# Kernel tuning notes

Measured on AMD Instinct MI355X. Metric: run time of the kernel, lower is better.

## Reference

```python
import jax, jax.numpy as jnp
import numpy as np

DX, DZ, DT = 10.0, 10.0, 1.0e-3
NX, NZ = 512, 512
NSTEPS, NREC = 512, 128
DT2 = DT * DT
INV_DXDZ = 1.0 / (DX * DZ)


def setup_inputs() -> dict:
    key = jax.random.key(0)
    k1, k2, k3, k4 = jax.random.split(key, 4)
    # velocity in [1500, 2500] m/s -> CFL stable with dt=1e-3, dx=dz=10
    velocity_model = 1500.0 + 1000.0 * jax.random.uniform(k1, (NX, NZ), dtype=jnp.float32)
    source = jax.random.normal(k2, (NSTEPS,), dtype=jnp.float32)
    rec_x = jax.random.randint(k3, (NREC,), 0, NX)
    rec_z = jax.random.randint(k4, (NREC,), 0, NZ)
    return {
        "velocity_model": velocity_model,
        "source": source,
        "src_x": 256,
        "src_z": 8,
        "rec_x": rec_x,
        "rec_z": rec_z,
    }


def _laplacian(p):
    # 3x3 cross stencil with zero padding, scaled by 1/(dx*dz) -- identical to
    # F.conv2d(p, [[0,1,0],[1,-4,1],[0,1,0]]/(dx*dz), padding=1)
    pp = jnp.pad(p, 1)
    return (pp[:-2, 1:-1] + pp[2:, 1:-1] + pp[1:-1, :-2] + pp[1:-1, 2:] - 4.0 * p) * INV_DXDZ


def reference(velocity_model, source, src_x, src_z, rec_x, rec_z):
    v2_dt2 = velocity_model * velocity_model * DT2  # [nx, nz]

    def step(carry, s_t):
        p, p_old = carry
        p_new = 2.0 * p - p_old + v2_dt2 * _laplacian(p)
        p_new = p_new.at[src_x, src_z].add(s_t * DT2)
        return (p_new, p), p_new[rec_x, rec_z]  # gather all receivers at once

    p0 = jnp.zeros((NX, NZ), dtype=velocity_model.dtype)
    _, recs = jax.lax.scan(step, (p0, p0), source)  # recs: [n_steps, n_rec]
    return recs.T  # seismogram: [n_rec, n_steps]
```

## Files before the change

kernel.cpp:

```cpp
#include <hip/hip_runtime.h>


#define NXd 512
#define NZd 512
#define NSTEPSd 512
#define NRECd 128
#define DT2f 1.0e-6f
#define INVf 1.0e-2f
#define TBk 16
#define TIk 32
#define EXTk 64
#define NTILEk 16
#define PADk 16
#define PWk 544
#define LROWS 66

__device__ __forceinline__ float dpp_shr1(float x) {
    int v = __builtin_amdgcn_update_dpp(0, __builtin_bit_cast(int, x),
                                        0x138, 0xF, 0xF, false);
    return __builtin_bit_cast(float, v);
}
__device__ __forceinline__ float dpp_shl1(float x) {
    int v = __builtin_amdgcn_update_dpp(0, __builtin_bit_cast(int, x),
                                        0x130, 0xF, 0xF, false);
    return __builtin_bit_cast(float, v);
}

__global__ __launch_bounds__(256) void fdtd_init(const float* __restrict__ vel,
                                                 float2* __restrict__ PA,
                                                 float2* __restrict__ PB,
                                                 float* __restrict__ V2,
                                                 float* __restrict__ out) {
    int p = blockIdx.x * blockDim.x + threadIdx.x;
    if (p < PWk * PWk) {
        int px = p / PWk, pz = p - px * PWk;
        float v2 = 0.f;
        if (px >= PADk && px < PADk + NXd && pz >= PADk && pz < PADk + NZd) {
            float v = vel[(px - PADk) * NZd + (pz - PADk)];
            v2 = v * v * (DT2f * INVf);
        }
        PA[p] = make_float2(0.f, 0.f);
        PB[p] = make_float2(0.f, 0.f);
        V2[p] = v2;
    }
    if (p < NRECd * NSTEPSd) out[p] = 0.f;
}

__global__ __launch_bounds__(1024) void fdtd_tblock(
    const float* __restrict__ source,
    const int* __restrict__ src_x, const int* __restrict__ src_z,
    const int* __restrict__ rec_x, const int* __restrict__ rec_z,
    const float2* __restrict__ Pin, float2* __restrict__ Pout,
    const float* __restrict__ V2, float* __restrict__ out,
    int t0, int ibase)
{
    __shared__ float sb[2][LROWS * EXTk];

    const int tid = threadIdx.x;
    const int w   = tid >> 6;
    const int ez  = tid & 63;
    const int gx0 = (blockIdx.y + ibase) * TIk;
    const int gz0 = blockIdx.x * TIk;
    const int ox = gx0 - TBk, oz = gz0 - TBk;
    const int gz = oz + ez;

    const int pbase = (gx0 + 4 * w) * PWk + gz0 + ez;
    float2 co[4]; float rV2i[4];
    #pragma unroll
    for (int i = 0; i < 4; ++i) {
        co[i]   = Pin[pbase + i * PWk];
        rV2i[i] = V2[pbase + i * PWk];
    }

    const int sx = *src_x, sz = *src_z;
    {
        int dxm = max(0, max(ox - sx, sx - (ox + EXTk - 1)));
        int dzm = max(0, max(oz - sz, sz - (oz + EXTk - 1)));
        if (dxm + dzm > t0 + TBk + 1) return;
    }

    bool rOwn = false; int rIdx = 0;
    if (tid < NRECd) {
        int rx = rec_x[tid], rz = rec_z[tid];
        rOwn = (rx >= gx0 && rx < gx0 + TIk && rz >= gz0 && rz < gz0 + TIk);
        rIdx = (rx - ox + 1) * EXTk + (rz - oz);
    }

    float rCur[4], rOld[4];
    #pragma unroll
    for (int i = 0; i < 4; ++i) {
        rCur[i] = co[i].x; rOld[i] = co[i].y;
        sb[0][(4 * w + 1 + i) * EXTk + ez] = rCur[i];
    }
    if (w == 0) {
        sb[0][ez] = 0.f;
        sb[0][(LROWS - 1) * EXTk + ez] = 0.f;
        sb[1][ez] = 0.f;
        sb[1][(LROWS - 1) * EXTk + ez] = 0.f;
    }

    const int exs = sx - ox, ezs = sz - oz;
    const bool srcHere = (exs >= 0 && exs < EXTk && ezs >= 0 && ezs < EXTk) &&
                         (tid == (((exs >> 2) << 6) | ezs));
    float sv[TBk];
    if (srcHere) {
        #pragma unroll
        for (int s = 0; s < TBk; ++s) sv[s] = source[t0 + s] * DT2f;
    }

    __syncthreads();

    const int fbase = 4 * w * EXTk + ez;

    float rv[TBk];
    #pragma unroll
    for (int s = 0; s < TBk; ++s) {
        const float* cur = sb[s & 1];
        float* nxt = sb[(s & 1) ^ 1];
        const float up0 = cur[fbase];
        const float dn3 = cur[fbase + 5 * EXTk];
        float nv[4];
        #pragma unroll
        for (int i = 0; i < 4; ++i) {
            const float up = (i == 0) ? up0 : rCur[i - 1];
            const float dn = (i == 3) ? dn3 : rCur[i + 1];
            const float lf = dpp_shr1(rCur[i]);
            const float rt = dpp_shl1(rCur[i]);
            const float sum = (up + dn) + (lf + rt);
            const float t4 = __builtin_fmaf(-4.0f, rCur[i], sum);
            const float pm = __builtin_fmaf(2.0f, rCur[i], -rOld[i]);
            nv[i] = __builtin_fmaf(rV2i[i], t4, pm);
        }
        #pragma unroll
        for (int i = 0; i < 4; ++i) {
            rOld[i] = rCur[i];
            rCur[i] = nv[i];
            nxt[fbase + (1 + i) * EXTk] = nv[i];
        }
        if (srcHere) {
            #pragma unroll
            for (int i = 0; i < 4; ++i) {
                if (i == (exs & 3)) {
                    rCur[i] += sv[s];
                    nxt[(exs + 1) * EXTk + ezs] = rCur[i];
                }
            }
        }
        __syncthreads();
        if (rOwn) rv[s] = nxt[rIdx];
    }

    if (w >= 4 && w < 12 && ez >= TBk && ez < EXTk - TBk) {
        #pragma unroll
        for (int i = 0; i < 4; ++i)
            Pout[pbase + i * PWk] = make_float2(rCur[i], rOld[i]);
    }

    if (rOwn) {
        #pragma unroll
        for (int s = 0; s < TBk; ++s)
            out[tid * NSTEPSd + t0 + s] = rv[s];
    }
}

extern "C" void kernel_launch(void* const* d_in, const int* in_sizes, int n_in,
                              void* d_out, int out_size, void* d_ws, size_t ws_size,
                              hipStream_t stream) {
    const float* vel    = (const float*)d_in[0];
    const float* source = (const float*)d_in[1];
    const int*   src_x  = (const int*)d_in[2];
    const int*   src_z  = (const int*)d_in[3];
    const int*   rec_x  = (const int*)d_in[4];
    const int*   rec_z  = (const int*)d_in[5];
    float* out = (float*)d_out;

    const size_t FP = (size_t)PWk * PWk;
    float2* PA = (float2*)d_ws;
    float2* PB = PA + FP;
    float*  V2 = (float*)(PB + FP);

    fdtd_init<<<(PWk * PWk + 255) / 256, 256, 0, stream>>>(vel, PA, PB, V2, out);

    for (int k = 0; k < NSTEPSd / TBk; ++k) {
        const int R = 16 * k + TBk + 1 + 32;
        const int tneg = 209 - R;
        int ilo = tneg > 0 ? (tneg + 31) / 32 : 0;
        int ihi = (272 + R) / 32; if (ihi > 15) ihi = 15;
        int jhi = (24 + R) / 32;  if (jhi > 15) jhi = 15;

        const float2* Pin = (k & 1) ? PB : PA;
        float2* Pout      = (k & 1) ? PA : PB;
        dim3 grid(jhi + 1, ihi - ilo + 1);
        fdtd_tblock<<<grid, dim3(1024), 0, stream>>>(source, src_x, src_z,
                                                     rec_x, rec_z, Pin, Pout,
                                                     V2, out, 16 * k, ilo);
    }
}
```

Baseline: 362.3 us.

## Replace per-chunk launches with a persistent cooperative kernel using grid sync

```diff
diff --git a/kernel.cpp b/kernel.cpp
--- a/kernel.cpp
+++ b/kernel.cpp
@@ -1,4 +1,7 @@
 #include <hip/hip_runtime.h>
+#include <hip/hip_cooperative_groups.h>
+
+namespace cg = cooperative_groups;
 
 
 #define NXd 512
@@ -26,58 +29,59 @@
     return __builtin_bit_cast(float, v);
 }
 
-__global__ __launch_bounds__(256) void fdtd_init(const float* __restrict__ vel,
-                                                 float2* __restrict__ PA,
-                                                 float2* __restrict__ PB,
-                                                 float* __restrict__ V2,
-                                                 float* __restrict__ out) {
-    int p = blockIdx.x * blockDim.x + threadIdx.x;
-    if (p < PWk * PWk) {
-        int px = p / PWk, pz = p - px * PWk;
-        float v2 = 0.f;
-        if (px >= PADk && px < PADk + NXd && pz >= PADk && pz < PADk + NZd) {
-            float v = vel[(px - PADk) * NZd + (pz - PADk)];
-            v2 = v * v * (DT2f * INVf);
-        }
-        PA[p] = make_float2(0.f, 0.f);
-        PB[p] = make_float2(0.f, 0.f);
-        V2[p] = v2;
-    }
-    if (p < NRECd * NSTEPSd) out[p] = 0.f;
-}
-
-__global__ __launch_bounds__(1024) void fdtd_tblock(
-    const float* __restrict__ source,
+__global__ __launch_bounds__(1024) void fdtd_persist(
+    const float* __restrict__ vel, const float* __restrict__ source,
     const int* __restrict__ src_x, const int* __restrict__ src_z,
     const int* __restrict__ rec_x, const int* __restrict__ rec_z,
-    const float2* __restrict__ Pin, float2* __restrict__ Pout,
-    const float* __restrict__ V2, float* __restrict__ out,
-    int t0, int ibase)
+    float2* __restrict__ PA, float2* __restrict__ PB,
+    float* __restrict__ out)
 {
+    cg::grid_group gg = cg::this_grid();
     __shared__ float sb[2][LROWS * EXTk];
 
     const int tid = threadIdx.x;
     const int w   = tid >> 6;
     const int ez  = tid & 63;
-    const int gx0 = (blockIdx.y + ibase) * TIk;
+    const int gx0 = blockIdx.y * TIk;
     const int gz0 = blockIdx.x * TIk;
     const int ox = gx0 - TBk, oz = gz0 - TBk;
-    const int gz = oz + ez;
-
-    const int pbase = (gx0 + 4 * w) * PWk + gz0 + ez;
-    float2 co[4]; float rV2i[4];
-    #pragma unroll
-    for (int i = 0; i < 4; ++i) {
-        co[i]   = Pin[pbase + i * PWk];
-        rV2i[i] = V2[pbase + i * PWk];
+
+    {
+        const int gsz = (int)(gridDim.x * gridDim.y) * (int)blockDim.x;
+        int g = ((int)(blockIdx.y * gridDim.x + blockIdx.x)) * (int)blockDim.x + tid;
+        for (int p = g; p < PWk * PWk; p += gsz) {
+            PA[p] = make_float2(0.f, 0.f);
+            PB[p] = make_float2(0.f, 0.f);
+        }
+        if (g < NRECd * NSTEPSd) out[g] = 0.f;
+    }
+
+    float rV2i[4];
+    {
+        const int fz = oz + ez;
+        #pragma unroll
+        for (int i = 0; i < 4; ++i) {
+            const int fx = ox + 4 * w + i;
+            float v2 = 0.f;
+            if (fx >= 0 && fx < NXd && fz >= 0 && fz < NZd) {
+                float v = vel[fx * NZd + fz];
+                v2 = v * v * (DT2f * INVf);
+            }
+            rV2i[i] = v2;
+        }
+    }
+
+    if (w == 0) {
+        sb[0][ez] = 0.f;
+        sb[0][(LROWS - 1) * EXTk + ez] = 0.f;
+        sb[1][ez] = 0.f;
+        sb[1][(LROWS - 1) * EXTk + ez] = 0.f;
     }
 
     const int sx = *src_x, sz = *src_z;
-    {
-        int dxm = max(0, max(ox - sx, sx - (ox + EXTk - 1)));
-        int dzm = max(0, max(oz - sz, sz - (oz + EXTk - 1)));
-        if (dxm + dzm > t0 + TBk + 1) return;
-    }
+    const int exs = sx - ox, ezs = sz - oz;
+    const bool srcHere = (exs >= 0 && exs < EXTk && ezs >= 0 && ezs < EXTk) &&
+                         (tid == (((exs >> 2) << 6) | ezs));
 
     bool rOwn = false; int rIdx = 0;
     if (tid < NRECd) {
@@ -86,80 +90,91 @@
         rIdx = (rx - ox + 1) * EXTk + (rz - oz);
     }
 
-    float rCur[4], rOld[4];
-    #pragma unroll
-    for (int i = 0; i < 4; ++i) {
-        rCur[i] = co[i].x; rOld[i] = co[i].y;
-        sb[0][(4 * w + 1 + i) * EXTk + ez] = rCur[i];
-    }
-    if (w == 0) {
-        sb[0][ez] = 0.f;
-        sb[0][(LROWS - 1) * EXTk + ez] = 0.f;
-        sb[1][ez] = 0.f;
-        sb[1][(LROWS - 1) * EXTk + ez] = 0.f;
-    }
-
-    const int exs = sx - ox, ezs = sz - oz;
-    const bool srcHere = (exs >= 0 && exs < EXTk && ezs >= 0 && ezs < EXTk) &&
-                         (tid == (((exs >> 2) << 6) | ezs));
-    float sv[TBk];
-    if (srcHere) {
-        #pragma unroll
-        for (int s = 0; s < TBk; ++s) sv[s] = source[t0 + s] * DT2f;
-    }
-
-    __syncthreads();
-
+    const int dxm = max(0, max(ox - sx, sx - (ox + EXTk - 1)));
+    const int dzm = max(0, max(oz - sz, sz - (oz + EXTk - 1)));
+    const int dman = dxm + dzm;
+
+    const int pbase = (gx0 + 4 * w) * PWk + gz0 + ez;
     const int fbase = 4 * w * EXTk + ez;
 
-    float rv[TBk];
-    #pragma unroll
-    for (int s = 0; s < TBk; ++s) {
-        const float* cur = sb[s & 1];
-        float* nxt = sb[(s & 1) ^ 1];
-        const float up0 = cur[fbase];
-        const float dn3 = cur[fbase + 5 * EXTk];
-        float nv[4];
-        #pragma unroll
-        for (int i = 0; i < 4; ++i) {
-            const float up = (i == 0) ? up0 : rCur[i - 1];
-            const float dn = (i == 3) ? dn3 : rCur[i + 1];
-            const float lf = dpp_shr1(rCur[i]);
-            const float rt = dpp_shl1(rCur[i]);
-            const float sum = (up + dn) + (lf + rt);
-            const float t4 = __builtin_fmaf(-4.0f, rCur[i], sum);
-            const float pm = __builtin_fmaf(2.0f, rCur[i], -rOld[i]);
-            nv[i] = __builtin_fmaf(rV2i[i], t4, pm);
-        }
-        #pragma unroll
-        for (int i = 0; i < 4; ++i) {
-            rOld[i] = rCur[i];
-            rCur[i] = nv[i];
-            nxt[fbase + (1 + i) * EXTk] = nv[i];
-        }
-        if (srcHere) {
+    gg.sync();
+
+    for (int k = 0; k < NSTEPSd / TBk; ++k) {
+        const int t0 = TBk * k;
+        if (dman <= t0 + TBk + 1) {
+            const float2* __restrict__ Pin = (k & 1) ? PB : PA;
+            float2*       __restrict__ Pout = (k & 1) ? PA : PB;
+
+            float2 co[4];
+            #pragma unroll
+            for (int i = 0; i < 4; ++i) co[i] = Pin[pbase + i * PWk];
+
+            float rCur[4], rOld[4];
             #pragma unroll
             for (int i = 0; i < 4; ++i) {
-                if (i == (exs & 3)) {
-                    rCur[i] += sv[s];
-                    nxt[(exs + 1) * EXTk + ezs] = rCur[i];
+                rCur[i] = co[i].x; rOld[i] = co[i].y;
+                sb[0][(4 * w + 1 + i) * EXTk + ez] = rCur[i];
+            }
+
+            float sv[TBk];
+            if (srcHere) {
+                #pragma unroll
+                for (int s = 0; s < TBk; ++s) sv[s] = source[t0 + s] * DT2f;
+            }
+
+            __syncthreads();
+
+            float rv[TBk];
+            #pragma unroll
+            for (int s = 0; s < TBk; ++s) {
+                const float* cur = sb[s & 1];
+                float* nxt = sb[(s & 1) ^ 1];
+                const float up0 = cur[fbase];
+                const float dn3 = cur[fbase + 5 * EXTk];
+                float nv[4];
+                #pragma unroll
+                for (int i = 0; i < 4; ++i) {
+                    const float up = (i == 0) ? up0 : rCur[i - 1];
+                    const float dn = (i == 3) ? dn3 : rCur[i + 1];
+                    const float lf = dpp_shr1(rCur[i]);
+                    const float rt = dpp_shl1(rCur[i]);
+                    const float sum = (up + dn) + (lf + rt);
+                    const float t4 = __builtin_fmaf(-4.0f, rCur[i], sum);
+                    const float pm = __builtin_fmaf(2.0f, rCur[i], -rOld[i]);
+                    nv[i] = __builtin_fmaf(rV2i[i], t4, pm);
                 }
+                #pragma unroll
+                for (int i = 0; i < 4; ++i) {
+                    rOld[i] = rCur[i];
+                    rCur[i] = nv[i];
+                    nxt[fbase + (1 + i) * EXTk] = nv[i];
+                }
+                if (srcHere) {
+                    #pragma unroll
+                    for (int i = 0; i < 4; ++i) {
+                        if (i == (exs & 3)) {
+                            rCur[i] += sv[s];
+                            nxt[(exs + 1) * EXTk + ezs] = rCur[i];
+                        }
+                    }
+                }
+                __syncthreads();
+                if (rOwn) rv[s] = nxt[rIdx];
+            }
+
+            if (w >= 4 && w < 12 && ez >= TBk && ez < EXTk - TBk) {
+                #pragma unroll
+                for (int i = 0; i < 4; ++i)
+                    Pout[pbase + i * PWk] = make_float2(rCur[i], rOld[i]);
+            }
+
+            if (rOwn) {
+                #pragma unroll
+                for (int s = 0; s < TBk; ++s)
+                    out[tid * NSTEPSd + t0 + s] = rv[s];
             }
         }
-        __syncthreads();
-        if (rOwn) rv[s] = nxt[rIdx];
-    }
-
-    if (w >= 4 && w < 12 && ez >= TBk && ez < EXTk - TBk) {
-        #pragma unroll
-        for (int i = 0; i < 4; ++i)
-            Pout[pbase + i * PWk] = make_float2(rCur[i], rOld[i]);
-    }
-
-    if (rOwn) {
-        #pragma unroll
-        for (int s = 0; s < TBk; ++s)
-            out[tid * NSTEPSd + t0 + s] = rv[s];
+        gg.sync();
     }
 }
 
@@ -177,22 +192,10 @@
     const size_t FP = (size_t)PWk * PWk;
     float2* PA = (float2*)d_ws;
     float2* PB = PA + FP;
-    float*  V2 = (float*)(PB + FP);
-
-    fdtd_init<<<(PWk * PWk + 255) / 256, 256, 0, stream>>>(vel, PA, PB, V2, out);
-
-    for (int k = 0; k < NSTEPSd / TBk; ++k) {
-        const int R = 16 * k + TBk + 1 + 32;
-        const int tneg = 209 - R;
-        int ilo = tneg > 0 ? (tneg + 31) / 32 : 0;
-        int ihi = (272 + R) / 32; if (ihi > 15) ihi = 15;
-        int jhi = (24 + R) / 32;  if (jhi > 15) jhi = 15;
-
-        const float2* Pin = (k & 1) ? PB : PA;
-        float2* Pout      = (k & 1) ? PA : PB;
-        dim3 grid(jhi + 1, ihi - ilo + 1);
-        fdtd_tblock<<<grid, dim3(1024), 0, stream>>>(source, src_x, src_z,
-                                                     rec_x, rec_z, Pin, Pout,
-                                                     V2, out, 16 * k, ilo);
-    }
-}
+
+    void* args[] = {(void*)&vel, (void*)&source, (void*)&src_x, (void*)&src_z,
+                    (void*)&rec_x, (void*)&rec_z, (void*)&PA, (void*)&PB,
+                    (void*)&out};
+    hipLaunchCooperativeKernel((void*)fdtd_persist, dim3(NTILEk, NTILEk),
+                               dim3(1024), args, 0, stream);
+}
```

New measurement: 1.107 ms. +205.4%, slower.
